# Optimization experiments

Measured on AMD Instinct MI355X. Metric: run time of the kernel, lower is better.

Reference implementation:

```python
import jax, jax.numpy as jnp
import numpy as np

N, M, K, CIN, COUT = 65536, 16385, 16, 256, 512
RATIO = 0.25
LN_EPS = 1e-5


def setup_inputs() -> dict:
    key = jax.random.key(0)
    k0, k1, k2, k3, k4 = jax.random.split(key, 5)
    xyz = jax.random.normal(k0, (N, 3), dtype=jnp.float32)
    feats = jax.random.normal(k1, (N, CIN), dtype=jnp.float32)
    samp_idx = jax.random.randint(k2, (M,), 0, N, dtype=jnp.int32)
    knn_idx = jax.random.randint(k3, (M, K), 0, N, dtype=jnp.int32)
    norm_w = jnp.ones((CIN,), dtype=jnp.float32)
    norm_b = jnp.zeros((CIN,), dtype=jnp.float32)
    lin_w = jax.random.normal(k4, (COUT, CIN), dtype=jnp.float32) * (1.0 / np.sqrt(CIN))
    return {"xyz": xyz, "feats": feats, "norm_w": norm_w, "norm_b": norm_b,
            "lin_w": lin_w, "samp_idx": samp_idx, "knn_idx": knn_idx, "offset": N}


def reference(xyz, feats, norm_w, norm_b, lin_w, samp_idx, knn_idx, offset):
    # n_offset = int(offset * ratio) + 1 (single point cloud)
    m = int(offset * RATIO) + 1
    n_offset = jnp.array([m], dtype=jnp.int32)
    # FPS output -> sampled coordinates
    n_xyz = xyz[samp_idx]                                  # [m, 3]
    # queryandgroup(use_xyz=False): gather k-NN neighbor features
    g = feats[knn_idx]                                     # [m, k, cin]
    # LayerNorm over channel dim
    mu = jnp.mean(g, axis=-1, keepdims=True)
    var = jnp.mean(jnp.square(g - mu), axis=-1, keepdims=True)
    normed = (g - mu) * jax.lax.rsqrt(var + LN_EPS) * norm_w + norm_b
    # bias-free Linear cin -> cout
    proj = jnp.einsum('mkc,oc->mko', normed, lin_w)        # [m, k, cout]
    # MaxPool1d over the k neighbors
    out = jnp.max(proj, axis=1)                            # [m, cout]
    return n_xyz, out, n_offset
```

## Files before the change

### kernel.cpp

```cpp
#include <hip/hip_runtime.h>

#define M_PTS   16385
#define K_NB    16
#define CIN_C   256
#define COUT_C  512
#define N_ROWS  65536
#define LN_EPS  1e-5f

#define OUT_XYZ_ELEMS (M_PTS * 3)
#define OUT_FEAT_OFF  OUT_XYZ_ELEMS
#define OUT_NOFF_IDX  (OUT_XYZ_ELEMS + M_PTS * COUT_C)

#define LN_BLOCKS   2048
#define PREP_BLOCKS 512

#define NBLK 513
#define PPB  32

#define B_SCALE 16.0f
#define B_INV   0.0625f
#define SCL_ONE 0x7F7F7F7F

#define AROW_B 272

typedef __attribute__((ext_vector_type(4))) float f32x4;
typedef __attribute__((ext_vector_type(8))) int   i32x8;
typedef __attribute__((ext_vector_type(2))) unsigned int uint2v;

__device__ __forceinline__ float wave_sum64(float v) {
  v += __int_as_float(__builtin_amdgcn_update_dpp(0, __float_as_int(v), 0xB1, 0xF, 0xF, false));
  v += __int_as_float(__builtin_amdgcn_update_dpp(0, __float_as_int(v), 0x4E, 0xF, 0xF, false));
  v += __int_as_float(__builtin_amdgcn_update_dpp(0, __float_as_int(v), 0x141, 0xF, 0xF, false));
  v += __int_as_float(__builtin_amdgcn_update_dpp(0, __float_as_int(v), 0x140, 0xF, 0xF, false));
  v += __int_as_float(__builtin_amdgcn_update_dpp(0, __float_as_int(v), 0x142, 0xA, 0xF, false));
  v += __int_as_float(__builtin_amdgcn_update_dpp(0, __float_as_int(v), 0x143, 0xC, 0xF, false));
  return __int_as_float(__builtin_amdgcn_readlane(__float_as_int(v), 63));
}

__device__ __forceinline__ int ln_pack(float4 g, float4 nw, float4 nb) {
  float s1 = (g.x + g.y) + (g.z + g.w);
  float s2 = g.x * g.x + g.y * g.y + g.z * g.z + g.w * g.w;
  float S1 = wave_sum64(s1);
  float S2 = wave_sum64(s2);
  float mu  = S1 * (1.0f / 256.0f);
  float var = fmaf(-mu, mu, S2 * (1.0f / 256.0f));
  float rs  = rsqrtf(var + LN_EPS);
  float a = fmaf((g.x - mu) * rs, nw.x, nb.x);
  float b = fmaf((g.y - mu) * rs, nw.y, nb.y);
  float c = fmaf((g.z - mu) * rs, nw.z, nb.z);
  float d = fmaf((g.w - mu) * rs, nw.w, nb.w);
  int v = __builtin_amdgcn_cvt_pk_fp8_f32(a, b, 0, false);
  v = __builtin_amdgcn_cvt_pk_fp8_f32(c, d, v, true);
  return v;
}

__global__ void prep_kernel(const float* __restrict__ lin_w,
                            const float* __restrict__ xyz,
                            const float* __restrict__ feats,
                            const float* __restrict__ norm_w,
                            const float* __restrict__ norm_b,
                            const int*   __restrict__ samp_idx,
                            const int*   __restrict__ offset,
                            unsigned char* __restrict__ lw8,
                            unsigned char* __restrict__ tab,
                            float*  __restrict__ out) {
  int bx = blockIdx.x;
  if (bx < LN_BLOCKS) {
    const int lane = threadIdx.x & 63;
    const int gw   = (bx << 2) + (threadIdx.x >> 6);
    const float4 nw = ((const float4*)norm_w)[lane];
    const float4 nb = ((const float4*)norm_b)[lane];
    const float4* f4 = (const float4*)feats;
    const int wo = lane << 2;
#pragma unroll
    for (int i = 0; i < 4; ++i) {
      const int ra = (i << 14) + (gw << 1);
      float4 ga = f4[(size_t)ra * 64 + lane];
      float4 gb = f4[(size_t)(ra + 1) * 64 + lane];
      int pka = ln_pack(ga, nw, nb);
      int pkb = ln_pack(gb, nw, nb);
      *(int*)(tab + ((size_t)ra << 8) + wo)       = pka;
      *(int*)(tab + ((size_t)(ra + 1) << 8) + wo) = pkb;
    }
    return;
  }
  int tid = (bx - LN_BLOCKS) * 256 + threadIdx.x;
  if (tid < COUT_C * CIN_C) {
    int o = tid >> 8;
    int c = tid & 255;
    int lanei = (((c >> 5) & 3) << 4) | (o & 15);
    int pos = ((o >> 5) << 13) | (((o >> 4) & 1) << 12) | ((c >> 7) << 11)
            | (lanei << 5) | (c & 31);
    int pk = __builtin_amdgcn_cvt_pk_fp8_f32(lin_w[tid] * B_SCALE, 0.0f, 0, false);
    lw8[pos] = (unsigned char)(pk & 0xFF);
  }
  if (tid < OUT_XYZ_ELEMS) {
    int p = tid / 3;
    int c = tid - p * 3;
    out[tid] = xyz[(size_t)samp_idx[p] * 3 + c];
  }
  if (tid == 0) out[OUT_NOFF_IDX] = (float)(offset[0] / 4 + 1);
}

__device__ __forceinline__ void load_row(const unsigned char* __restrict__ src,
                                         unsigned char* ldsrow) {
  __builtin_amdgcn_global_load_lds(
      (const __attribute__((address_space(1))) unsigned int*)src,
      (__attribute__((address_space(3))) unsigned int*)ldsrow,
      4, 0, 0);
}

__device__ __forceinline__ float pool16(f32x4 a) {
  float v = fmaxf(fmaxf(a[0], a[1]), fmaxf(a[2], a[3]));
  uint2v r = __builtin_amdgcn_permlane16_swap(__float_as_uint(v), __float_as_uint(v), false, false);
  v = fmaxf(__uint_as_float(r.x), __uint_as_float(r.y));
  uint2v s = __builtin_amdgcn_permlane32_swap(__float_as_uint(v), __float_as_uint(v), false, false);
  return fmaxf(__uint_as_float(s.x), __uint_as_float(s.y));
}

__device__ __forceinline__ void gemm_pool(const unsigned char* rowbase,
                                          const i32x8 Breg[2][2],
                                          float& v0, float& v1) {
  i32x8 ak0 = *(const i32x8*)(rowbase);
  i32x8 ak1 = *(const i32x8*)(rowbase + 128);
  f32x4 a0 = {0.f, 0.f, 0.f, 0.f}, a1 = {0.f, 0.f, 0.f, 0.f};
  a0 = __builtin_amdgcn_mfma_scale_f32_16x16x128_f8f6f4(
         ak0, Breg[0][0], a0, 0, 0, 0, SCL_ONE, 0, SCL_ONE);
  a1 = __builtin_amdgcn_mfma_scale_f32_16x16x128_f8f6f4(
         ak0, Breg[1][0], a1, 0, 0, 0, SCL_ONE, 0, SCL_ONE);
  a0 = __builtin_amdgcn_mfma_scale_f32_16x16x128_f8f6f4(
         ak1, Breg[0][1], a0, 0, 0, 0, SCL_ONE, 0, SCL_ONE);
  a1 = __builtin_amdgcn_mfma_scale_f32_16x16x128_f8f6f4(
         ak1, Breg[1][1], a1, 0, 0, 0, SCL_ONE, 0, SCL_ONE);
  v0 = pool16(a0);
  v1 = pool16(a1);
}

__global__ __launch_bounds__(1024, 8)
void td_main(const unsigned char* __restrict__ tab,
             const unsigned char* __restrict__ lw8,
             const int*    __restrict__ knn,
             float* __restrict__ out) {
  __shared__ __align__(16) unsigned char A8[4][32][AROW_B];
  __shared__ int Kidx[PPB * K_NB];

  const int tid  = threadIdx.x;
  const int lane = tid & 63;
  const int w    = tid >> 6;
  const int quad = lane >> 4;
  const int lcol = lane & 15;

  const int pstart = blockIdx.x * PPB;
  const int npts   = min(pstart + PPB, M_PTS) - pstart;
  if (npts <= 0) return;

  for (int i = tid; i < npts * K_NB; i += 1024)
    Kidx[i] = knn[pstart * K_NB + i] << 8;

  i32x8 Breg[2][2];
  {
    const unsigned char* base = lw8 + (w << 13) + lane * 32;
#pragma unroll
    for (int g = 0; g < 2; ++g)
#pragma unroll
      for (int ks = 0; ks < 2; ++ks) {
        Breg[g][ks] = *(const i32x8*)(base + (g << 12) + (ks << 11));
        asm volatile("" : "+v"(Breg[g][ks]));
      }
  }

  const unsigned char* tabL = tab + (lane << 2);

  __syncthreads();

  load_row(tabL + (unsigned)Kidx[w],                           &A8[0][w][0]);
  load_row(tabL + (unsigned)Kidx[min(1, npts - 1) * K_NB + w], &A8[0][16 + w][0]);

  const int nit = (npts + 1) >> 1;
  for (int it = 0; it < nit; ++it) {
    const int pa = 2 * it, pb = 2 * it + 1;

    if (it + 1 < nit) {
      int qa = min(pa + 2, npts - 1), qb = min(pa + 3, npts - 1);
      int b = (it + 1) & 3;
      load_row(tabL + (unsigned)Kidx[qa * K_NB + w], &A8[b][w][0]);
      load_row(tabL + (unsigned)Kidx[qb * K_NB + w], &A8[b][16 + w][0]);
    }

    if (it == 0) {
      if (nit > 1) asm volatile("s_waitcnt vmcnt(2)" ::: "memory");
      else         asm volatile("s_waitcnt vmcnt(0)" ::: "memory");
    } else if (it + 1 < nit) {
      asm volatile("s_waitcnt vmcnt(3)" ::: "memory");
    } else {
      asm volatile("s_waitcnt vmcnt(1)" ::: "memory");
    }
    __builtin_amdgcn_s_barrier();

    const unsigned char* Ab = &A8[it & 3][0][0];
    const unsigned char* rowb = Ab + lcol * AROW_B + quad * 32;

    float v0, v1;
    gemm_pool(rowb, Breg, v0, v1);
    float* outa = out + OUT_FEAT_OFF + (size_t)(pstart + pa) * COUT_C + w * 32;
    if (quad < 2) outa[quad * 16 + lcol] = (quad ? v1 : v0) * B_INV;

    gemm_pool(rowb + 16 * AROW_B, Breg, v0, v1);
    if (pb < npts) {
      float* outb = out + OUT_FEAT_OFF + (size_t)(pstart + pb) * COUT_C + w * 32;
      if (quad < 2) outb[quad * 16 + lcol] = (quad ? v1 : v0) * B_INV;
    }
  }
}

extern "C" void kernel_launch(void* const* d_in, const int* in_sizes, int n_in,
                              void* d_out, int out_size, void* d_ws, size_t ws_size,
                              hipStream_t stream) {
  const float* xyz      = (const float*)d_in[0];
  const float* feats    = (const float*)d_in[1];
  const float* norm_w   = (const float*)d_in[2];
  const float* norm_b   = (const float*)d_in[3];
  const float* lin_w    = (const float*)d_in[4];
  const int*   samp_idx = (const int*)d_in[5];
  const int*   knn      = (const int*)d_in[6];
  const int*   offset   = (const int*)d_in[7];
  float* out = (float*)d_out;
  unsigned char* lw8 = (unsigned char*)d_ws;
  unsigned char* tab = (unsigned char*)d_ws + (1 << 17);

  prep_kernel<<<LN_BLOCKS + PREP_BLOCKS, 256, 0, stream>>>(
      lin_w, xyz, feats, norm_w, norm_b, samp_idx, offset, lw8, tab, out);

  td_main<<<NBLK, 1024, 0, stream>>>(tab, lw8, knn, out);
}
```

Measured before the change: 148.4 us.

## Halve block to 512 threads with each wave covering 64 output channels

Each wave now computes 64 output channels instead of 32, holding four B fragments in registers. The block shrinks from 16 waves to 8, and each wave loads two neighbor rows per point instead of one. This spreads the gathered A tile over more MFMAs per wave and cuts per-wave overhead such as barriers, pooling permutes and stores, which are now fully used across all lanes. The cost is higher register pressure from eight i32x8 B fragments and fewer waves to hide gather latency.

```diff
diff --git a/kernel.cpp b/kernel.cpp
--- a/kernel.cpp
+++ b/kernel.cpp
@@ -89,7 +89,7 @@
     int o = tid >> 8;
     int c = tid & 255;
     int lanei = (((c >> 5) & 3) << 4) | (o & 15);
-    int pos = ((o >> 5) << 13) | (((o >> 4) & 1) << 12) | ((c >> 7) << 11)
+    int pos = ((o >> 6) << 14) | (((o >> 4) & 3) << 12) | ((c >> 7) << 11)
             | (lanei << 5) | (c & 31);
     int pk = __builtin_amdgcn_cvt_pk_fp8_f32(lin_w[tid] * B_SCALE, 0.0f, 0, false);
     lw8[pos] = (unsigned char)(pk & 0xFF);
@@ -118,25 +118,36 @@
   return fmaxf(__uint_as_float(s.x), __uint_as_float(s.y));
 }
 
-__device__ __forceinline__ void gemm_pool(const unsigned char* rowbase,
-                                          const i32x8 Breg[2][2],
-                                          float& v0, float& v1) {
+__device__ __forceinline__ float gemm_pool64(const unsigned char* rowbase,
+                                             const i32x8 Breg[4][2], int quad) {
   i32x8 ak0 = *(const i32x8*)(rowbase);
   i32x8 ak1 = *(const i32x8*)(rowbase + 128);
   f32x4 a0 = {0.f, 0.f, 0.f, 0.f}, a1 = {0.f, 0.f, 0.f, 0.f};
+  f32x4 a2 = {0.f, 0.f, 0.f, 0.f}, a3 = {0.f, 0.f, 0.f, 0.f};
   a0 = __builtin_amdgcn_mfma_scale_f32_16x16x128_f8f6f4(
          ak0, Breg[0][0], a0, 0, 0, 0, SCL_ONE, 0, SCL_ONE);
   a1 = __builtin_amdgcn_mfma_scale_f32_16x16x128_f8f6f4(
          ak0, Breg[1][0], a1, 0, 0, 0, SCL_ONE, 0, SCL_ONE);
+  a2 = __builtin_amdgcn_mfma_scale_f32_16x16x128_f8f6f4(
+         ak0, Breg[2][0], a2, 0, 0, 0, SCL_ONE, 0, SCL_ONE);
+  a3 = __builtin_amdgcn_mfma_scale_f32_16x16x128_f8f6f4(
+         ak0, Breg[3][0], a3, 0, 0, 0, SCL_ONE, 0, SCL_ONE);
   a0 = __builtin_amdgcn_mfma_scale_f32_16x16x128_f8f6f4(
          ak1, Breg[0][1], a0, 0, 0, 0, SCL_ONE, 0, SCL_ONE);
   a1 = __builtin_amdgcn_mfma_scale_f32_16x16x128_f8f6f4(
          ak1, Breg[1][1], a1, 0, 0, 0, SCL_ONE, 0, SCL_ONE);
-  v0 = pool16(a0);
-  v1 = pool16(a1);
-}
-
-__global__ __launch_bounds__(1024, 8)
+  a2 = __builtin_amdgcn_mfma_scale_f32_16x16x128_f8f6f4(
+         ak1, Breg[2][1], a2, 0, 0, 0, SCL_ONE, 0, SCL_ONE);
+  a3 = __builtin_amdgcn_mfma_scale_f32_16x16x128_f8f6f4(
+         ak1, Breg[3][1], a3, 0, 0, 0, SCL_ONE, 0, SCL_ONE);
+  float v0 = pool16(a0);
+  float v1 = pool16(a1);
+  float v2 = pool16(a2);
+  float v3 = pool16(a3);
+  return (quad == 0) ? v0 : (quad == 1) ? v1 : (quad == 2) ? v2 : v3;
+}
+
+__global__ __launch_bounds__(512, 4)
 void td_main(const unsigned char* __restrict__ tab,
              const unsigned char* __restrict__ lw8,
              const int*    __restrict__ knn,
@@ -154,14 +165,14 @@
   const int npts   = min(pstart + PPB, M_PTS) - pstart;
   if (npts <= 0) return;
 
-  for (int i = tid; i < npts * K_NB; i += 1024)
+  for (int i = tid; i < npts * K_NB; i += 512)
     Kidx[i] = knn[pstart * K_NB + i] << 8;
 
-  i32x8 Breg[2][2];
+  i32x8 Breg[4][2];
   {
-    const unsigned char* base = lw8 + (w << 13) + lane * 32;
+    const unsigned char* base = lw8 + (w << 14) + lane * 32;
 #pragma unroll
-    for (int g = 0; g < 2; ++g)
+    for (int g = 0; g < 4; ++g)
 #pragma unroll
       for (int ks = 0; ks < 2; ++ks) {
         Breg[g][ks] = *(const i32x8*)(base + (g << 12) + (ks << 11));
@@ -173,8 +184,13 @@
 
   __syncthreads();
 
-  load_row(tabL + (unsigned)Kidx[w],                           &A8[0][w][0]);
-  load_row(tabL + (unsigned)Kidx[min(1, npts - 1) * K_NB + w], &A8[0][16 + w][0]);
+  {
+    int p1 = min(1, npts - 1);
+    load_row(tabL + (unsigned)Kidx[w],                 &A8[0][w][0]);
+    load_row(tabL + (unsigned)Kidx[8 + w],             &A8[0][8 + w][0]);
+    load_row(tabL + (unsigned)Kidx[p1 * K_NB + w],     &A8[0][16 + w][0]);
+    load_row(tabL + (unsigned)Kidx[p1 * K_NB + 8 + w], &A8[0][24 + w][0]);
+  }
 
   const int nit = (npts + 1) >> 1;
   for (int it = 0; it < nit; ++it) {
@@ -183,32 +199,33 @@
     if (it + 1 < nit) {
       int qa = min(pa + 2, npts - 1), qb = min(pa + 3, npts - 1);
       int b = (it + 1) & 3;
-      load_row(tabL + (unsigned)Kidx[qa * K_NB + w], &A8[b][w][0]);
-      load_row(tabL + (unsigned)Kidx[qb * K_NB + w], &A8[b][16 + w][0]);
+      load_row(tabL + (unsigned)Kidx[qa * K_NB + w],     &A8[b][w][0]);
+      load_row(tabL + (unsigned)Kidx[qa * K_NB + 8 + w], &A8[b][8 + w][0]);
+      load_row(tabL + (unsigned)Kidx[qb * K_NB + w],     &A8[b][16 + w][0]);
+      load_row(tabL + (unsigned)Kidx[qb * K_NB + 8 + w], &A8[b][24 + w][0]);
     }
 
     if (it == 0) {
-      if (nit > 1) asm volatile("s_waitcnt vmcnt(2)" ::: "memory");
+      if (nit > 1) asm volatile("s_waitcnt vmcnt(4)" ::: "memory");
       else         asm volatile("s_waitcnt vmcnt(0)" ::: "memory");
     } else if (it + 1 < nit) {
-      asm volatile("s_waitcnt vmcnt(3)" ::: "memory");
+      asm volatile("s_waitcnt vmcnt(6)" ::: "memory");
     } else {
-      asm volatile("s_waitcnt vmcnt(1)" ::: "memory");
+      asm volatile("s_waitcnt vmcnt(2)" ::: "memory");
     }
     __builtin_amdgcn_s_barrier();
 
     const unsigned char* Ab = &A8[it & 3][0][0];
     const unsigned char* rowb = Ab + lcol * AROW_B + quad * 32;
 
-    float v0, v1;
-    gemm_pool(rowb, Breg, v0, v1);
-    float* outa = out + OUT_FEAT_OFF + (size_t)(pstart + pa) * COUT_C + w * 32;
-    if (quad < 2) outa[quad * 16 + lcol] = (quad ? v1 : v0) * B_INV;
-
-    gemm_pool(rowb + 16 * AROW_B, Breg, v0, v1);
+    float va = gemm_pool64(rowb, Breg, quad);
+    float* outa = out + OUT_FEAT_OFF + (size_t)(pstart + pa) * COUT_C + w * 64;
+    outa[lane] = va * B_INV;
+
+    float vb = gemm_pool64(rowb + 16 * AROW_B, Breg, quad);
     if (pb < npts) {
-      float* outb = out + OUT_FEAT_OFF + (size_t)(pstart + pb) * COUT_C + w * 32;
-      if (quad < 2) outb[quad * 16 + lcol] = (quad ? v1 : v0) * B_INV;
+      float* outb = out + OUT_FEAT_OFF + (size_t)(pstart + pb) * COUT_C + w * 64;
+      outb[lane] = vb * B_INV;
     }
   }
 }
@@ -231,5 +248,5 @@
   prep_kernel<<<LN_BLOCKS + PREP_BLOCKS, 256, 0, stream>>>(
       lin_w, xyz, feats, norm_w, norm_b, samp_idx, offset, lw8, tab, out);
 
-  td_main<<<NBLK, 1024, 0, stream>>>(tab, lw8, knn, out);
-}
+  td_main<<<NBLK, 512, 0, stream>>>(tab, lw8, knn, out);
+}
```

After: 150.9 us. No clear change (+1.7%).
